# Performance work log

Hardware: AMD Instinct MI355X
Metric: run time of the kernel (lower is better)

## Reference

```python
import jax, jax.numpy as jnp
import numpy as np

NUM_HEADS = 16
NUM_KV_HEADS = 4
ROPE_BASE = 10000.0
TRAIN_SEQ_LEN = 2048


def _rms_norm(x):
    eps = jnp.asarray(jnp.finfo(x.dtype).eps, x.dtype)
    return x * jax.lax.rsqrt(jnp.mean(x * x, axis=-1, keepdims=True) + eps)


def _rope_cos_sin(seq_len, head_dim, dtype):
    # seq_len <= TRAIN_SEQ_LEN -> no NTK rescaling, matches Rotary buffer path
    half = head_dim // 2
    inv_freq = 1.0 / (ROPE_BASE ** (jnp.arange(0, head_dim, 2, dtype=jnp.float32) / head_dim))
    t = jnp.arange(seq_len, dtype=jnp.float32)
    freqs = jnp.outer(t, inv_freq)  # [S, half]
    cos = jnp.cos(freqs)[None, :, None, :].astype(dtype)
    sin = jnp.sin(freqs)[None, :, None, :].astype(dtype)
    return cos, sin


def _apply_rotary(x, cos, sin):
    half = x.shape[-1] // 2
    x1, x2 = x[..., :half], x[..., half:]
    return jnp.concatenate([x1 * cos + x2 * sin, -x1 * sin + x2 * cos], axis=-1)


def setup_inputs() -> dict:
    key = jax.random.key(0)
    ks = jax.random.split(key, 5)
    B, S, D = 2, 2048, 2048
    kv_dim = NUM_KV_HEADS * (D // NUM_HEADS)
    sw = 0.02
    return {
        "x": jax.random.normal(ks[0], (B, S, D), jnp.float32),
        "Wq": jax.random.normal(ks[1], (D, D), jnp.float32) * sw,
        "Wk": jax.random.normal(ks[2], (kv_dim, D), jnp.float32) * sw,
        "Wv": jax.random.normal(ks[3], (kv_dim, D), jnp.float32) * sw,
        "Wproj": jax.random.normal(ks[4], (D, D), jnp.float32) * sw,
        "q_gain": jnp.ones((NUM_HEADS,), jnp.float32),
    }


def reference(x, Wq, Wk, Wv, Wproj, q_gain):
    B, S, D = x.shape
    H, Hkv = NUM_HEADS, NUM_KV_HEADS
    hd = D // H
    r = H // Hkv

    q = (x @ Wq.T).reshape(B, S, H, hd)
    k = (x @ Wk.T).reshape(B, S, Hkv, hd)
    v = (x @ Wv.T).reshape(B, S, Hkv, hd)

    q = _rms_norm(q)
    k = _rms_norm(k)

    cos, sin = _rope_cos_sin(S, hd, q.dtype)
    q = _apply_rotary(q, cos, sin)
    k = _apply_rotary(k, cos, sin)
    q = q * q_gain.astype(q.dtype)[None, None, :, None]

    # GQA: repeat kv heads (repeat_interleave along head dim)
    k = jnp.repeat(k, r, axis=2)  # [B,S,H,hd]
    v = jnp.repeat(v, r, axis=2)

    scale = 1.0 / jnp.sqrt(jnp.asarray(hd, q.dtype))
    scores = jnp.einsum("bqhd,bkhd->bhqk", q, k) * scale
    causal = jnp.tril(jnp.ones((S, S), dtype=bool))
    scores = jnp.where(causal[None, None], scores, jnp.asarray(-jnp.inf, scores.dtype))
    attn = jax.nn.softmax(scores, axis=-1)
    y = jnp.einsum("bhqk,bkhd->bqhd", attn, v)

    return y.reshape(B, S, D) @ Wproj.T
```

## Files before the change

kernel.cpp:

```cpp
#include <hip/hip_runtime.h>

#define D_MODEL 2048
#define SEQ 2048
#define BATCH 2
#define NH 16
#define NKV 4
#define HD 128
#define KVD (NKV * HD)
#define QKVN (D_MODEL + 2 * KVD)
#define MROWS (BATCH * SEQ)

typedef __attribute__((ext_vector_type(8))) short short8;
typedef __attribute__((ext_vector_type(4))) float f32x4;

__device__ __forceinline__ unsigned short f2bf(float f) {
    union { float f; unsigned int u; } v; v.f = f;
    unsigned int r = (v.u + 0x7FFFu + ((v.u >> 16) & 1u)) >> 16;
    return (unsigned short)r;
}

__device__ __forceinline__ unsigned short f2bf_pos(float f) {
    union { float f; unsigned int u; } v; v.f = f;
    return (unsigned short)((v.u + 0x8000u) >> 16);
}

__device__ __forceinline__ float bf2f(unsigned short u) {
    union { float f; unsigned int i; } v; v.i = ((unsigned int)u) << 16;
    return v.f;
}

__device__ __forceinline__ void async16(const void* g, void* l) {
    __builtin_amdgcn_global_load_lds((const __attribute__((address_space(1))) void*)g,
                                     (__attribute__((address_space(3))) void*)l, 16, 0, 0);
}

__global__ __launch_bounds__(256) void cast_all(const float* __restrict__ x,
                                                const float* __restrict__ wq,
                                                const float* __restrict__ wk,
                                                const float* __restrict__ wv,
                                                const float* __restrict__ wp,
                                                unsigned short* __restrict__ xb,
                                                unsigned short* __restrict__ wqkv,
                                                unsigned short* __restrict__ wpb) {
    int i = blockIdx.x * 256 + threadIdx.x;
    const float4* s; ushort4* d; int j;
    if (i < 2097152)      { s = (const float4*)x;  d = (ushort4*)xb;             j = i; }
    else if (i < 3145728) { s = (const float4*)wq; d = (ushort4*)wqkv;           j = i - 2097152; }
    else if (i < 3407872) { s = (const float4*)wk; d = (ushort4*)wqkv + 1048576; j = i - 3145728; }
    else if (i < 3670016) { s = (const float4*)wv; d = (ushort4*)wqkv + 1310720; j = i - 3407872; }
    else                  { s = (const float4*)wp; d = (ushort4*)wpb;            j = i - 3670016; }
    float4 v = s[j];
    ushort4 o;
    o.x = f2bf(v.x); o.y = f2bf(v.y); o.z = f2bf(v.z); o.w = f2bf(v.w);
    d[j] = o;
}

__global__ __launch_bounds__(512) void gemm_qkv(const unsigned short* __restrict__ A,
                                                const unsigned short* __restrict__ W,
                                                const float* __restrict__ gain,
                                                unsigned short* __restrict__ qbuf,
                                                unsigned short* __restrict__ kbuf,
                                                unsigned short* __restrict__ vtb) {
    __shared__ unsigned short smem[65536];
    unsigned short* tile = smem;
    const int K = D_MODEL;
    const int tid  = threadIdx.x;
    const int lane = tid & 63;
    const int wave = tid >> 6;
    const int qm   = lane & 15;
    const int quad = lane >> 4;
    const int wr   = wave >> 2;
    const int wc   = wave & 3;
    const int m0 = blockIdx.y * 256;
    const int bx = blockIdx.x;
    const int n0 = bx * 256;

    f32x4 acc[2][2][4][2];
#pragma unroll
    for (int a = 0; a < 2; a++)
#pragma unroll
        for (int b = 0; b < 2; b++)
#pragma unroll
            for (int c = 0; c < 4; c++)
#pragma unroll
                for (int d = 0; d < 2; d++) acc[a][b][c][d] = (f32x4){0.f, 0.f, 0.f, 0.f};

    const unsigned short* Asrc = A + (size_t)(m0 + (tid >> 3)) * K + (((tid & 7) ^ ((tid >> 3) & 7)) * 8);
    const unsigned short* Bsrc = W + (size_t)(n0 + (tid >> 3)) * K + (((tid & 7) ^ ((tid >> 3) & 7)) * 8);
    const int dstg = tid * 8;
    const int ck0 = ((quad ^ (qm & 7)) * 8);
    const int ck1 = (((4 + quad) ^ (qm & 7)) * 8);
    const int arow = wr * 64 + qm;
    const int brow = wc * 32 + qm;

    short8 af[4][2], bf0[2][2], bf1[2][2];

#define STG_A(mh, bufv, kt1) \
    async16(Asrc + (size_t)((mh) * 128) * K + (kt1),      &smem[(bufv) * 16384 + (mh) * 8192 + dstg]); \
    async16(Asrc + (size_t)((mh) * 128 + 64) * K + (kt1), &smem[(bufv) * 16384 + (mh) * 8192 + 4096 + dstg]);
#define STG_B(nh, bufv, kt1) \
    async16(Bsrc + (size_t)((nh) * 128) * K + (kt1),      &smem[32768 + (bufv) * 16384 + (nh) * 8192 + dstg]); \
    async16(Bsrc + (size_t)((nh) * 128 + 64) * K + (kt1), &smem[32768 + (bufv) * 16384 + (nh) * 8192 + 4096 + dstg]);

#define RD_A(ab, mh) { \
    _Pragma("unroll") \
    for (int m = 0; m < 4; m++) { \
        af[m][0] = *(const short8*)&smem[(ab) + ((mh) * 128 + arow + m * 16) * 64 + ck0]; \
        af[m][1] = *(const short8*)&smem[(ab) + ((mh) * 128 + arow + m * 16) * 64 + ck1]; \
    } }
#define RD_B(bb, nh, dstf) { \
    _Pragma("unroll") \
    for (int n = 0; n < 2; n++) { \
        dstf[n][0] = *(const short8*)&smem[(bb) + ((nh) * 128 + brow + n * 16) * 64 + ck0]; \
        dstf[n][1] = *(const short8*)&smem[(bb) + ((nh) * 128 + brow + n * 16) * 64 + ck1]; \
    } }
#define MFMA16(mh, nh, bfr) { \
    __builtin_amdgcn_s_setprio(1); \
    _Pragma("unroll") \
    for (int m = 0; m < 4; m++) \
        _Pragma("unroll") \
        for (int n = 0; n < 2; n++) { \
            acc[mh][nh][m][n] = __builtin_amdgcn_mfma_f32_16x16x32_bf16(af[m][0], bfr[n][0], acc[mh][nh][m][n], 0, 0, 0); \
            acc[mh][nh][m][n] = __builtin_amdgcn_mfma_f32_16x16x32_bf16(af[m][1], bfr[n][1], acc[mh][nh][m][n], 0, 0, 0); \
        } \
    __builtin_amdgcn_s_setprio(0); }

#define BARv asm volatile("s_barrier" ::: "memory")
#define WV4  asm volatile("s_waitcnt vmcnt(4)" ::: "memory")
#define WV2  asm volatile("s_waitcnt vmcnt(2)" ::: "memory")
#define WV0  asm volatile("s_waitcnt vmcnt(0)" ::: "memory")

#define STEP(p, kt1) { \
     RD_A((p)*16384, 0) RD_B(32768 + (p)*16384, 0, bf0) STG_A(0, (p)^1, kt1) \
    BARv; MFMA16(0, 0, bf0) WV4; BARv; \
     RD_B(32768 + (p)*16384, 1, bf1) STG_B(0, (p)^1, kt1) \
    BARv; MFMA16(0, 1, bf1) WV4; BARv; \
     RD_A((p)*16384, 1) STG_B(1, (p)^1, kt1) \
    BARv; MFMA16(1, 0, bf0) BARv; \
     STG_A(1, (p)^1, kt1) \
    BARv; MFMA16(1, 1, bf1) WV4; BARv; \
}
#define STEPE(p) { \
    RD_A((p)*16384, 0) RD_B(32768 + (p)*16384, 0, bf0) BARv; MFMA16(0, 0, bf0) WV2; BARv; \
    RD_B(32768 + (p)*16384, 1, bf1)                    BARv; MFMA16(0, 1, bf1) WV0; BARv; \
    RD_A((p)*16384, 1)                                 BARv; MFMA16(1, 0, bf0) BARv; \
    MFMA16(1, 1, bf1) \
}

    STG_A(0, 0, 0) STG_B(0, 0, 0) STG_B(1, 0, 0) STG_A(1, 0, 0)
    WV4; BARv;

#pragma unroll 1
    for (int t2 = 0; t2 < 15; ++t2) {
        STEP(0, t2 * 128 + 64)
        STEP(1, t2 * 128 + 128)
    }
    STEP(0, 1984)
    STEPE(1)
#undef STG_A
#undef STG_B
#undef RD_A
#undef RD_B
#undef MFMA16
#undef STEP
#undef STEPE

    const int s_base = m0 & 2047;
    const int bb = m0 >> 11;
    const float invf = __builtin_amdgcn_exp2f(-(float)lane * 0.20761871f - 2.6514961f);

#pragma unroll
    for (int half = 0; half < 2; ++half) {
        __syncthreads();
#pragma unroll
        for (int nh = 0; nh < 2; nh++)
#pragma unroll
            for (int m = 0; m < 4; m++)
#pragma unroll
                for (int n = 0; n < 2; n++)
#pragma unroll
                    for (int r = 0; r < 4; r++) {
                        int row = wr * 64 + m * 16 + quad * 4 + r;
                        int col = nh * 128 + wc * 32 + n * 16 + qm;
                        tile[row * 264 + col] = f2bf(acc[half][nh][m][n][r]);
                    }
        __syncthreads();

        if (bx < 10) {
            const bool isq = bx < 8;
#pragma unroll
            for (int hh = 0; hh < 2; hh++) {
                const int h = (isq ? 2 * bx : (bx - 8) * 2) + hh;
                const float g = isq ? gain[h] * 0.12751744f : 1.0f;
                unsigned short* dst = isq
                    ? qbuf + ((size_t)(bb * NH + h) * SEQ + s_base + half * 128) * HD
                    : kbuf + ((size_t)(bb * NKV + h) * SEQ + s_base + half * 128) * HD;
                for (int rr = 0; rr < 16; rr++) {
                    int row = wave * 16 + rr;
                    float x1 = bf2f(tile[row * 264 + hh * 128 + lane]);
                    float x2 = bf2f(tile[row * 264 + hh * 128 + 64 + lane]);
                    float ss = x1 * x1 + x2 * x2;
                    ss += __shfl_xor(ss, 1);  ss += __shfl_xor(ss, 2);  ss += __shfl_xor(ss, 4);
                    ss += __shfl_xor(ss, 8);  ss += __shfl_xor(ss, 16); ss += __shfl_xor(ss, 32);
                    float rs = rsqrtf(ss * (1.0f / 128.0f) + 1.1920929e-07f);
                    float rev = (float)(s_base + half * 128 + row) * invf;
                    rev -= truncf(rev);
                    float sn = __builtin_amdgcn_sinf(rev);
                    float cs = __builtin_amdgcn_cosf(rev);
                    float a1 = x1 * rs, a2 = x2 * rs;
                    float o1 = (a1 * cs + a2 * sn) * g;
                    float o2 = (a2 * cs - a1 * sn) * g;
                    dst[(size_t)row * HD + lane]      = f2bf(o1);
                    dst[(size_t)row * HD + 64 + lane] = f2bf(o2);
                }
            }
        } else {
            const int sc = (tid & 31) * 4;
            const int d0 = tid >> 5;
#pragma unroll
            for (int hh = 0; hh < 2; hh++) {
                const int hk = (bx - 10) * 2 + hh;
                unsigned short* dstv = vtb + ((size_t)(bb * NKV + hk) * HD) * SEQ + s_base + half * 128;
#pragma unroll
                for (int i = 0; i < 8; i++) {
                    int d = d0 + 16 * i;
                    ushort4 ov;
                    ov.x = tile[(sc + 0) * 264 + hh * 128 + d];
                    ov.y = tile[(sc + 1) * 264 + hh * 128 + d];
                    ov.z = tile[(sc + 2) * 264 + hh * 128 + d];
                    ov.w = tile[(sc + 3) * 264 + hh * 128 + d];
                    *(ushort4*)(dstv + (size_t)d * SEQ + sc) = ov;
                }
            }
        }
    }
}

__global__ __launch_bounds__(256) void gemm_bt(const unsigned short* __restrict__ A,
                                               const unsigned short* __restrict__ W,
                                               float* __restrict__ C, int M, int N, int K) {
    __shared__ unsigned short smem[16384];
    const int tid  = threadIdx.x;
    const int lane = tid & 63;
    const int wave = tid >> 6;
    const int qm   = lane & 15;
    const int quad = lane >> 4;
    const int m0 = blockIdx.y * 128;
    const int n0 = blockIdx.x * 128;
    const int wm = (wave >> 1) * 64;
    const int wn = (wave & 1) * 64;

    f32x4 acc[4][4];
#pragma unroll
    for (int i = 0; i < 4; i++)
#pragma unroll
        for (int j = 0; j < 4; j++) acc[i][j] = (f32x4){0.f, 0.f, 0.f, 0.f};

    const int r1 = tid >> 2;
    const int c1 = (((tid & 3) ^ ((tid >> 3) & 3)) * 8);
    const unsigned short* Ag = A + (size_t)(m0 + r1) * K + c1;
    const unsigned short* Wg = W + (size_t)(n0 + r1) * K + c1;
    const int stg = wave * 512;
    const int swq = ((qm >> 1) & 3) * 8;

#define STG_B(bufv) \
    async16(Ag,                  &smem[(bufv) * 4096 + stg]); \
    async16(Ag + (size_t)64 * K, &smem[(bufv) * 4096 + 2048 + stg]); \
    async16(Wg,                  &smem[8192 + (bufv) * 4096 + stg]); \
    async16(Wg + (size_t)64 * K, &smem[8192 + (bufv) * 4096 + 2048 + stg]); \
    Ag += 32; Wg += 32;

#define CMP_B(bufv) { \
    short8 af[4], bfr[4]; \
    _Pragma("unroll") \
    for (int i = 0; i < 4; i++) { \
        af[i]  = *(const short8*)&smem[(bufv) * 4096 + (wm + i * 16 + qm) * 32 + (quad * 8 ^ swq)]; \
        bfr[i] = *(const short8*)&smem[8192 + (bufv) * 4096 + (wn + i * 16 + qm) * 32 + (quad * 8 ^ swq)]; \
    } \
    __builtin_amdgcn_s_setprio(1); \
    _Pragma("unroll") \
    for (int mi = 0; mi < 4; mi++) \
        _Pragma("unroll") \
        for (int ni = 0; ni < 4; ni++) \
            acc[mi][ni] = __builtin_amdgcn_mfma_f32_16x16x32_bf16(af[mi], bfr[ni], acc[mi][ni], 0, 0, 0); \
    __builtin_amdgcn_s_setprio(0); \
}

    STG_B(0)
    for (int t = 0; t < 31; ++t) {
        STG_B(1)
        asm volatile("s_waitcnt vmcnt(4)\n\ts_barrier" ::: "memory");
        CMP_B(0)
        asm volatile("s_barrier" ::: "memory");
        STG_B(0)
        asm volatile("s_waitcnt vmcnt(4)\n\ts_barrier" ::: "memory");
        CMP_B(1)
        asm volatile("s_barrier" ::: "memory");
    }
    STG_B(1)
    asm volatile("s_waitcnt vmcnt(4)\n\ts_barrier" ::: "memory");
    CMP_B(0)
    asm volatile("s_waitcnt vmcnt(0)\n\ts_barrier" ::: "memory");
    CMP_B(1)
#undef STG_B
#undef CMP_B

#pragma unroll
    for (int mi = 0; mi < 4; mi++) {
#pragma unroll
        for (int r = 0; r < 4; r++) {
            int row = m0 + wm + mi * 16 + quad * 4 + r;
            float* Crow = C + (size_t)row * N + n0 + wn + qm;
#pragma unroll
            for (int ni = 0; ni < 4; ni++) Crow[ni * 16] = acc[mi][ni][r];
        }
    }
}

__global__ __launch_bounds__(256, 4) void attn(const unsigned short* __restrict__ qb,
                                               const unsigned short* __restrict__ kb,
                                               const unsigned short* __restrict__ vt,
                                               const float* __restrict__ gain,
                                               unsigned short* __restrict__ y) {
    __shared__ unsigned short Ks[8192];
    __shared__ unsigned short Vs[8192];
    __shared__ unsigned short plds[4][1024];
    const int tid  = threadIdx.x;
    const int lane = tid & 63;
    const int wave = tid >> 6;
    const int bh   = blockIdx.x & 31;
    const int g4   = blockIdx.x >> 5;
    const int gg = g4 & 7;
    const int gs = g4 >> 3;
    const int qt64 = (gs == 0) ? gg : (gs == 1) ? (31 - gg) : (gs == 2) ? (8 + gg) : (23 - gg);
    const int h = bh & 15;
    const int b = bh >> 4;
    const int qm   = lane & 15;
    const int quad = lane >> 4;
    const int q0    = qt64 * 64;
    const int qrow0 = q0 + wave * 16;
    const float M = 17.0f * fabsf(gain[h]);

    const unsigned short* Qp = qb + (((size_t)(b * NH + h)) * SEQ + qrow0) * HD;
    const unsigned short* Kp = kb + ((size_t)(b * NKV + (h >> 2))) * SEQ * HD;
    const unsigned short* Vp = vt + ((size_t)(b * NKV + (h >> 2))) * HD * SEQ;

    short8 qf[4];
#pragma unroll
    for (int c = 0; c < 4; c++)
        qf[c] = *(const short8*)(Qp + qm * HD + c * 32 + quad * 8);

    f32x4 o[8];
#pragma unroll
    for (int t = 0; t < 8; t++) o[t] = (f32x4){0.f, 0.f, 0.f, 0.f};
    float lr[4] = {0.f, 0.f, 0.f, 0.f};

    const unsigned short* KsA = Kp + (size_t)(tid >> 4) * HD + (((tid & 15) ^ (tid >> 4)) & 15) * 8;
    const unsigned short* VsA = Vp + (size_t)(tid >> 3) * SEQ + (((tid & 7) ^ ((tid >> 3) & 7)) * 8);
    char* KsB = (char*)Ks + wave * 1024;
    char* VsB = (char*)Vs + wave * 1024;
    unsigned short* P = &plds[wave][0];

    const int kvend = q0 + 64;
    for (int kv0 = 0; kv0 < kvend; kv0 += 64) {
#pragma unroll
        for (int i = 0; i < 4; i++) {
            async16(KsA + (size_t)(16 * i) * HD,  KsB + i * 4096);
            async16(VsA + (size_t)(32 * i) * SEQ, VsB + i * 4096);
        }
        KsA += (size_t)64 * HD;
        VsA += 64;
        __syncthreads();

        f32x4 s[4];
#pragma unroll
        for (int g = 0; g < 4; g++) s[g] = (f32x4){0.f, 0.f, 0.f, 0.f};
#pragma unroll
        for (int c = 0; c < 4; c++) {
#pragma unroll
            for (int g = 0; g < 4; g++) {
                short8 kf = *(const short8*)&Ks[(g * 16 + qm) * 128 + (((c * 4 + quad) ^ qm) * 8)];
                s[g] = __builtin_amdgcn_mfma_f32_16x16x32_bf16(qf[c], kf, s[g], 0, 0, 0);
            }
        }
        if (kv0 + 63 > qrow0) {
#pragma unroll
            for (int g = 0; g < 4; g++)
#pragma unroll
                for (int r = 0; r < 4; r++) {
                    int qg = qrow0 + quad * 4 + r;
                    if (kv0 + g * 16 + qm > qg) s[g][r] = -3.0e38f;
                }
        }
        float p[4][4];
#pragma unroll
        for (int g = 0; g < 4; g++)
#pragma unroll
            for (int r = 0; r < 4; r++) {
                p[g][r] = __builtin_amdgcn_exp2f(s[g][r] - M);
                lr[r] += p[g][r];
            }
#pragma unroll
        for (int g = 0; g < 4; g++)
#pragma unroll
            for (int r = 0; r < 4; r++) {
                int rowp = quad * 4 + r;
                P[rowp * 64 + (((g * 2 + (qm >> 3)) ^ (rowp & 7)) * 8) + (qm & 7)] = f2bf_pos(p[g][r]);
            }
        short8 pa[2];
#pragma unroll
        for (int ka = 0; ka < 2; ka++)
            pa[ka] = *(const short8*)&P[qm * 64 + (((ka * 4 + quad) ^ (qm & 7)) * 8)];
#pragma unroll
        for (int t = 0; t < 8; t++) {
#pragma unroll
            for (int ka = 0; ka < 2; ka++) {
                short8 vf = *(const short8*)&Vs[(t * 16 + qm) * 64 + (((ka * 4 + quad) ^ (qm & 7)) * 8)];
                o[t] = __builtin_amdgcn_mfma_f32_16x16x32_bf16(pa[ka], vf, o[t], 0, 0, 0);
            }
        }
        __syncthreads();
    }
    float rl[4];
#pragma unroll
    for (int r = 0; r < 4; r++) {
        float l = lr[r];
        l += __shfl_xor(l, 1);
        l += __shfl_xor(l, 2);
        l += __shfl_xor(l, 4);
        l += __shfl_xor(l, 8);
        rl[r] = 1.0f / l;
    }
#pragma unroll
    for (int t = 0; t < 8; t++) {
#pragma unroll
        for (int r = 0; r < 4; r++) {
            size_t row = (size_t)(b * SEQ + qrow0 + quad * 4 + r);
            y[row * D_MODEL + h * HD + t * 16 + qm] = f2bf(o[t][r] * rl[r]);
        }
    }
}

extern "C" void kernel_launch(void* const* d_in, const int* in_sizes, int n_in,
                              void* d_out, int out_size, void* d_ws, size_t ws_size,
                              hipStream_t stream) {
    const float* x  = (const float*)d_in[0];
    const float* Wq = (const float*)d_in[1];
    const float* Wk = (const float*)d_in[2];
    const float* Wv = (const float*)d_in[3];
    const float* Wp = (const float*)d_in[4];
    const float* qg = (const float*)d_in[5];

    char* ws = (char*)d_ws;
    unsigned short* xb   = (unsigned short*)(ws + 0);
    unsigned short* wqkv = (unsigned short*)(ws + 16777216);
    unsigned short* wp   = (unsigned short*)(ws + 29360128);
    unsigned short* qbuf = (unsigned short*)(ws + 37748736);
    unsigned short* kbuf = (unsigned short*)(ws + 54525952);
    unsigned short* vtb  = (unsigned short*)(ws + 58720256);
    unsigned short* y    = xb;

    cast_all<<<18432, 256, 0, stream>>>(x, Wq, Wk, Wv, Wp, xb, wqkv, wp);
    gemm_qkv<<<dim3(12, 16), 512, 0, stream>>>(xb, wqkv, qg, qbuf, kbuf, vtb);
    attn<<<1024, 256, 0, stream>>>(qbuf, kbuf, vtb, qg, y);
    gemm_bt<<<dim3(16, 32), 256, 0, stream>>>(y, wp, (float*)d_out, MROWS, D_MODEL, D_MODEL);
}
```

Baseline: 285.8 us.

## Double-buffer K/V tiles in attention and swizzle QKV GEMM block order

The attention kernel now keeps two K/V LDS buffers and prefetches the next 64-key tile while computing on the current one. Explicit vmcnt waits and raw barriers replace __syncthreads, which hides global-load latency behind MFMA work. This doubles K/V LDS use and lowers the occupancy hint from 4 to 2 blocks per CU. Separately, the QKV GEMM remaps block indices into a grouped order so blocks that run at the same time share A/W tiles in cache.

Result: no change. 287.6 us (+0.6%).

```diff
diff --git a/kernel.cpp b/kernel.cpp
--- a/kernel.cpp
+++ b/kernel.cpp
@@ -71,8 +71,10 @@
     const int quad = lane >> 4;
     const int wr   = wave >> 2;
     const int wc   = wave & 3;
-    const int m0 = blockIdx.y * 256;
-    const int bx = blockIdx.x;
+    const int lin = blockIdx.x + 12 * blockIdx.y;
+    const int l2  = (lin & 7) * 24 + (lin >> 3);
+    const int bx  = l2 % 12;
+    const int m0  = (l2 / 12) * 256;
     const int n0 = bx * 256;
 
     f32x4 acc[2][2][4][2];
@@ -263,14 +265,14 @@
     const int stg = wave * 512;
     const int swq = ((qm >> 1) & 3) * 8;
 
-#define STG_B(bufv) \
+#define STG_B2(bufv) \
     async16(Ag,                  &smem[(bufv) * 4096 + stg]); \
     async16(Ag + (size_t)64 * K, &smem[(bufv) * 4096 + 2048 + stg]); \
     async16(Wg,                  &smem[8192 + (bufv) * 4096 + stg]); \
     async16(Wg + (size_t)64 * K, &smem[8192 + (bufv) * 4096 + 2048 + stg]); \
     Ag += 32; Wg += 32;
 
-#define CMP_B(bufv) { \
+#define CMP_B2(bufv) { \
     short8 af[4], bfr[4]; \
     _Pragma("unroll") \
     for (int i = 0; i < 4; i++) { \
@@ -286,24 +288,24 @@
     __builtin_amdgcn_s_setprio(0); \
 }
 
-    STG_B(0)
+    STG_B2(0)
     for (int t = 0; t < 31; ++t) {
-        STG_B(1)
+        STG_B2(1)
         asm volatile("s_waitcnt vmcnt(4)\n\ts_barrier" ::: "memory");
-        CMP_B(0)
+        CMP_B2(0)
         asm volatile("s_barrier" ::: "memory");
-        STG_B(0)
+        STG_B2(0)
         asm volatile("s_waitcnt vmcnt(4)\n\ts_barrier" ::: "memory");
-        CMP_B(1)
+        CMP_B2(1)
         asm volatile("s_barrier" ::: "memory");
     }
-    STG_B(1)
+    STG_B2(1)
     asm volatile("s_waitcnt vmcnt(4)\n\ts_barrier" ::: "memory");
-    CMP_B(0)
+    CMP_B2(0)
     asm volatile("s_waitcnt vmcnt(0)\n\ts_barrier" ::: "memory");
-    CMP_B(1)
-#undef STG_B
-#undef CMP_B
+    CMP_B2(1)
+#undef STG_B2
+#undef CMP_B2
 
 #pragma unroll
     for (int mi = 0; mi < 4; mi++) {
@@ -317,13 +319,13 @@
     }
 }
 
-__global__ __launch_bounds__(256, 4) void attn(const unsigned short* __restrict__ qb,
+__global__ __launch_bounds__(256, 2) void attn(const unsigned short* __restrict__ qb,
                                                const unsigned short* __restrict__ kb,
                                                const unsigned short* __restrict__ vt,
                                                const float* __restrict__ gain,
                                                unsigned short* __restrict__ y) {
-    __shared__ unsigned short Ks[8192];
-    __shared__ unsigned short Vs[8192];
+    __shared__ unsigned short Ks[2][8192];
+    __shared__ unsigned short Vs[2][8192];
     __shared__ unsigned short plds[4][1024];
     const int tid  = threadIdx.x;
     const int lane = tid & 63;
@@ -357,20 +359,32 @@
 
     const unsigned short* KsA = Kp + (size_t)(tid >> 4) * HD + (((tid & 15) ^ (tid >> 4)) & 15) * 8;
     const unsigned short* VsA = Vp + (size_t)(tid >> 3) * SEQ + (((tid & 7) ^ ((tid >> 3) & 7)) * 8);
-    char* KsB = (char*)Ks + wave * 1024;
-    char* VsB = (char*)Vs + wave * 1024;
+    char* KsB = (char*)&Ks[0][0] + wave * 1024;
+    char* VsB = (char*)&Vs[0][0] + wave * 1024;
     unsigned short* P = &plds[wave][0];
 
+#define STG_KV(pp) { \
+    _Pragma("unroll") \
+    for (int i = 0; i < 4; i++) { \
+        async16(KsA + (size_t)(16 * i) * HD,  KsB + (pp) * 16384 + i * 4096); \
+        async16(VsA + (size_t)(32 * i) * SEQ, VsB + (pp) * 16384 + i * 4096); \
+    } \
+    KsA += (size_t)64 * HD; \
+    VsA += 64; }
+
     const int kvend = q0 + 64;
+    STG_KV(0)
+    int p = 0;
     for (int kv0 = 0; kv0 < kvend; kv0 += 64) {
-#pragma unroll
-        for (int i = 0; i < 4; i++) {
-            async16(KsA + (size_t)(16 * i) * HD,  KsB + i * 4096);
-            async16(VsA + (size_t)(32 * i) * SEQ, VsB + i * 4096);
-        }
-        KsA += (size_t)64 * HD;
-        VsA += 64;
-        __syncthreads();
+        if (kv0 + 64 < kvend) {
+            STG_KV(p ^ 1)
+            asm volatile("s_waitcnt vmcnt(8)" ::: "memory");
+        } else {
+            asm volatile("s_waitcnt vmcnt(0)" ::: "memory");
+        }
+        __builtin_amdgcn_s_barrier();
+        const unsigned short* Ksp = &Ks[p][0];
+        const unsigned short* Vsp = &Vs[p][0];
 
         f32x4 s[4];
 #pragma unroll
@@ -379,7 +393,7 @@
         for (int c = 0; c < 4; c++) {
 #pragma unroll
             for (int g = 0; g < 4; g++) {
-                short8 kf = *(const short8*)&Ks[(g * 16 + qm) * 128 + (((c * 4 + quad) ^ qm) * 8)];
+                short8 kf = *(const short8*)&Ksp[(g * 16 + qm) * 128 + (((c * 4 + quad) ^ qm) * 8)];
                 s[g] = __builtin_amdgcn_mfma_f32_16x16x32_bf16(qf[c], kf, s[g], 0, 0, 0);
             }
         }
@@ -392,20 +406,20 @@
                     if (kv0 + g * 16 + qm > qg) s[g][r] = -3.0e38f;
                 }
         }
-        float p[4][4];
+        float pv[4][4];
 #pragma unroll
         for (int g = 0; g < 4; g++)
 #pragma unroll
             for (int r = 0; r < 4; r++) {
-                p[g][r] = __builtin_amdgcn_exp2f(s[g][r] - M);
-                lr[r] += p[g][r];
+                pv[g][r] = __builtin_amdgcn_exp2f(s[g][r] - M);
+                lr[r] += pv[g][r];
             }
 #pragma unroll
         for (int g = 0; g < 4; g++)
 #pragma unroll
             for (int r = 0; r < 4; r++) {
                 int rowp = quad * 4 + r;
-                P[rowp * 64 + (((g * 2 + (qm >> 3)) ^ (rowp & 7)) * 8) + (qm & 7)] = f2bf_pos(p[g][r]);
+                P[rowp * 64 + (((g * 2 + (qm >> 3)) ^ (rowp & 7)) * 8) + (qm & 7)] = f2bf_pos(pv[g][r]);
             }
         short8 pa[2];
 #pragma unroll
@@ -415,12 +429,14 @@
         for (int t = 0; t < 8; t++) {
 #pragma unroll
             for (int ka = 0; ka < 2; ka++) {
-                short8 vf = *(const short8*)&Vs[(t * 16 + qm) * 64 + (((ka * 4 + quad) ^ (qm & 7)) * 8)];
+                short8 vf = *(const short8*)&Vsp[(t * 16 + qm) * 64 + (((ka * 4 + quad) ^ (qm & 7)) * 8)];
                 o[t] = __builtin_amdgcn_mfma_f32_16x16x32_bf16(pa[ka], vf, o[t], 0, 0, 0);
             }
         }
-        __syncthreads();
-    }
+        __builtin_amdgcn_s_barrier();
+        p ^= 1;
+    }
+#undef STG_KV
     float rl[4];
 #pragma unroll
     for (int r = 0; r < 4; r++) {
```

## Deepen gemm_bt LDS pipeline to 64-wide K stages and swizzle QKV block order

Applied to the files above, without the earlier changes.

The output-projection GEMM now double-buffers 64-element K stages split into two 32-wide halves. Each half is prefetched for the next buffer while the current half is computed, which removes the extra barrier per step and overlaps loads with MFMA work. This doubles LDS use per block, which may reduce occupancy. The QKV GEMM also remaps block indices in a grouped order so that blocks running at the same time share A/W tiles in L2.

Result: no change. 284.8 us (-0.4%).

```diff
diff --git a/kernel.cpp b/kernel.cpp
--- a/kernel.cpp
+++ b/kernel.cpp
@@ -71,8 +71,10 @@
     const int quad = lane >> 4;
     const int wr   = wave >> 2;
     const int wc   = wave & 3;
-    const int m0 = blockIdx.y * 256;
-    const int bx = blockIdx.x;
+    const int lin = blockIdx.x + 12 * blockIdx.y;
+    const int l2  = (lin & 7) * 24 + (lin >> 3);
+    const int bx  = l2 % 12;
+    const int m0  = (l2 / 12) * 256;
     const int n0 = bx * 256;
 
     f32x4 acc[2][2][4][2];
@@ -239,7 +241,9 @@
 __global__ __launch_bounds__(256) void gemm_bt(const unsigned short* __restrict__ A,
                                                const unsigned short* __restrict__ W,
                                                float* __restrict__ C, int M, int N, int K) {
-    __shared__ unsigned short smem[16384];
+    __shared__ unsigned short smem[32768];
+    unsigned short* Al = smem;
+    unsigned short* Bl = smem + 16384;
     const int tid  = threadIdx.x;
     const int lane = tid & 63;
     const int wave = tid >> 6;
@@ -263,19 +267,18 @@
     const int stg = wave * 512;
     const int swq = ((qm >> 1) & 3) * 8;
 
-#define STG_B(bufv) \
-    async16(Ag,                  &smem[(bufv) * 4096 + stg]); \
-    async16(Ag + (size_t)64 * K, &smem[(bufv) * 4096 + 2048 + stg]); \
-    async16(Wg,                  &smem[8192 + (bufv) * 4096 + stg]); \
-    async16(Wg + (size_t)64 * K, &smem[8192 + (bufv) * 4096 + 2048 + stg]); \
-    Ag += 32; Wg += 32;
-
-#define CMP_B(bufv) { \
+#define STG_B2(khv, bufv) \
+    async16(Ag + (khv) * 32,                  &Al[(bufv) * 8192 + (khv) * 4096 + stg]); \
+    async16(Ag + (khv) * 32 + (size_t)64 * K, &Al[(bufv) * 8192 + (khv) * 4096 + 2048 + stg]); \
+    async16(Wg + (khv) * 32,                  &Bl[(bufv) * 8192 + (khv) * 4096 + stg]); \
+    async16(Wg + (khv) * 32 + (size_t)64 * K, &Bl[(bufv) * 8192 + (khv) * 4096 + 2048 + stg]);
+
+#define CMP_B2(bufv, khv) { \
     short8 af[4], bfr[4]; \
     _Pragma("unroll") \
     for (int i = 0; i < 4; i++) { \
-        af[i]  = *(const short8*)&smem[(bufv) * 4096 + (wm + i * 16 + qm) * 32 + (quad * 8 ^ swq)]; \
-        bfr[i] = *(const short8*)&smem[8192 + (bufv) * 4096 + (wn + i * 16 + qm) * 32 + (quad * 8 ^ swq)]; \
+        af[i]  = *(const short8*)&Al[(bufv) * 8192 + (khv) * 4096 + (wm + i * 16 + qm) * 32 + (quad * 8 ^ swq)]; \
+        bfr[i] = *(const short8*)&Bl[(bufv) * 8192 + (khv) * 4096 + (wn + i * 16 + qm) * 32 + (quad * 8 ^ swq)]; \
     } \
     __builtin_amdgcn_s_setprio(1); \
     _Pragma("unroll") \
@@ -286,24 +289,27 @@
     __builtin_amdgcn_s_setprio(0); \
 }
 
-    STG_B(0)
-    for (int t = 0; t < 31; ++t) {
-        STG_B(1)
+    STG_B2(0, 0)
+    STG_B2(1, 0)
+    Ag += 64; Wg += 64;
+    asm volatile("s_waitcnt vmcnt(4)\n\ts_barrier" ::: "memory");
+
+    int buf = 0;
+    for (int t = 0; t < K / 64 - 1; ++t) {
+        STG_B2(0, buf ^ 1)
+        CMP_B2(buf, 0)
         asm volatile("s_waitcnt vmcnt(4)\n\ts_barrier" ::: "memory");
-        CMP_B(0)
-        asm volatile("s_barrier" ::: "memory");
-        STG_B(0)
+        STG_B2(1, buf ^ 1)
+        CMP_B2(buf, 1)
         asm volatile("s_waitcnt vmcnt(4)\n\ts_barrier" ::: "memory");
-        CMP_B(1)
-        asm volatile("s_barrier" ::: "memory");
-    }
-    STG_B(1)
-    asm volatile("s_waitcnt vmcnt(4)\n\ts_barrier" ::: "memory");
-    CMP_B(0)
+        Ag += 64; Wg += 64;
+        buf ^= 1;
+    }
+    CMP_B2(buf, 0)
     asm volatile("s_waitcnt vmcnt(0)\n\ts_barrier" ::: "memory");
-    CMP_B(1)
-#undef STG_B
-#undef CMP_B
+    CMP_B2(buf, 1)
+#undef STG_B2
+#undef CMP_B2
 
 #pragma unroll
     for (int mi = 0; mi < 4; mi++) {
```
